# Optimization experiments

Measured on AMD Instinct MI355X. Metric: run time of the kernel, lower is better.

Reference implementation:

```python
import jax, jax.numpy as jnp
import numpy as np


def setup_inputs() -> dict:
    key = jax.random.key(0)
    ks = jax.random.split(key, 8)
    N, E = 100000, 3200000
    IN, H, OUT = 256, 128, 64
    x = jax.random.normal(ks[0], (N, IN), dtype=jnp.float32)
    src = jax.random.randint(ks[1], (E,), 0, N, dtype=jnp.int64)
    dst = jax.random.randint(ks[2], (E,), 0, N, dtype=jnp.int64)
    # Glorot-ish scaled weights
    W1_self = jax.random.normal(ks[3], (IN, H), dtype=jnp.float32) / np.sqrt(IN)
    W1_neigh = jax.random.normal(ks[4], (IN, H), dtype=jnp.float32) / np.sqrt(IN)
    b1 = jnp.zeros((H,), dtype=jnp.float32)
    W2_self = jax.random.normal(ks[5], (H, OUT), dtype=jnp.float32) / np.sqrt(H)
    W2_neigh = jax.random.normal(ks[6], (H, OUT), dtype=jnp.float32) / np.sqrt(H)
    b2 = jnp.zeros((OUT,), dtype=jnp.float32)
    return {"x": x, "src": src, "dst": dst,
            "W1_self": W1_self, "W1_neigh": W1_neigh, "b1": b1,
            "W2_self": W2_self, "W2_neigh": W2_neigh, "b2": b2}


def _sage_mean(h, src, dst, W_self, W_neigh, b, deg_inv):
    # mean aggregation over in-neighbors (edges src -> dst)
    N = h.shape[0]
    agg = jax.ops.segment_sum(h[src], dst, num_segments=N)  # [N, F]
    h_neigh = agg * deg_inv[:, None]
    return h @ W_self + h_neigh @ W_neigh + b


def reference(x, src, dst, W1_self, W1_neigh, b1, W2_self, W2_neigh, b2):
    N = x.shape[0]
    deg = jax.ops.segment_sum(jnp.ones_like(dst, dtype=x.dtype), dst, num_segments=N)
    deg_inv = 1.0 / jnp.maximum(deg, 1.0)  # DGL clamps in-degree to >= 1
    h = _sage_mean(x, src, dst, W1_self, W1_neigh, b1, deg_inv)
    h = jax.nn.relu(h)
    h = _sage_mean(h, src, dst, W2_self, W2_neigh, b2, deg_inv)
    return h
```

## Files before the change

kernel.cpp:

```cpp
#include <hip/hip_runtime.h>
#include <hip/hip_bf16.h>


typedef unsigned int uint32;
typedef __attribute__((ext_vector_type(8))) short short8;
typedef __attribute__((ext_vector_type(4))) float f32x4;

#define NBMAX 1024
#define EPB   8192

__device__ __forceinline__ unsigned short f2bf(float f) {
    unsigned u = __float_as_uint(f);
    u += 0x7fffu + ((u >> 16) & 1u);
    return (unsigned short)(u >> 16);
}
__device__ __forceinline__ uint32 pack2bf(float lo, float hi) {
    return (uint32)f2bf(lo) | ((uint32)f2bf(hi) << 16);
}
__device__ __forceinline__ float bf_lo(uint32 v) { return __uint_as_float(v << 16); }
__device__ __forceinline__ float bf_hi(uint32 v) { return __uint_as_float(v & 0xFFFF0000u); }

__global__ __launch_bounds__(256) void k_bucket_count(const int* __restrict__ dst, int E,
                                                      int* __restrict__ bcnt) {
    __shared__ int hist[NBMAX];
    for (int i = threadIdx.x; i < NBMAX; i += 256) hist[i] = 0;
    __syncthreads();
    int base = blockIdx.x * EPB;
    #pragma unroll 4
    for (int i = 0; i < EPB / 256; ++i) {
        int e = base + i * 256 + threadIdx.x;
        if (e < E) atomicAdd(&hist[dst[e] >> 7], 1);
    }
    __syncthreads();
    for (int i = threadIdx.x; i < NBMAX; i += 256) {
        int h = hist[i];
        if (h) atomicAdd(&bcnt[i], h);
    }
}

__global__ __launch_bounds__(1024) void k_bucket_scan(const int* __restrict__ bcnt, int NB,
                                                      int* __restrict__ boffs, int* __restrict__ gfill,
                                                      int E) {
    __shared__ int sd[1024];
    int tid = threadIdx.x;
    int v = (tid < NB) ? bcnt[tid] : 0;
    sd[tid] = v;
    __syncthreads();
    for (int off = 1; off < 1024; off <<= 1) {
        int t = (tid >= off) ? sd[tid - off] : 0;
        __syncthreads();
        sd[tid] += t;
        __syncthreads();
    }
    int excl = sd[tid] - v;
    if (tid < NB) { boffs[tid] = excl; gfill[tid] = excl; }
    if (tid == 0) boffs[NB] = E;
}

__global__ __launch_bounds__(256) void k_bucket_scatter(const int* __restrict__ src,
                                                        const int* __restrict__ dst, int E,
                                                        int* __restrict__ gfill,
                                                        uint32* __restrict__ pairs) {
    __shared__ int hist[NBMAX];
    __shared__ int basea[NBMAX];
    for (int i = threadIdx.x; i < NBMAX; i += 256) hist[i] = 0;
    __syncthreads();
    int base = blockIdx.x * EPB;
    #pragma unroll 4
    for (int i = 0; i < EPB / 256; ++i) {
        int e = base + i * 256 + threadIdx.x;
        if (e < E) atomicAdd(&hist[dst[e] >> 7], 1);
    }
    __syncthreads();
    for (int i = threadIdx.x; i < NBMAX; i += 256) {
        int h = hist[i];
        basea[i] = h ? atomicAdd(&gfill[i], h) : 0;
        hist[i] = 0;
    }
    __syncthreads();
    #pragma unroll 4
    for (int i = 0; i < EPB / 256; ++i) {
        int e = base + i * 256 + threadIdx.x;
        if (e < E) {
            int d = dst[e];
            int b = d >> 7;
            int pos = basea[b] + atomicAdd(&hist[b], 1);
            pairs[pos] = ((uint32)src[e] << 7) | (uint32)(d & 127);
        }
    }
}

__global__ __launch_bounds__(256) void k_bucket_sort(const uint32* __restrict__ pairs,
                                                     const int* __restrict__ boffs,
                                                     int N, int E,
                                                     int* __restrict__ row_start,
                                                     float* __restrict__ deg_inv,
                                                     int* __restrict__ src_sorted) {
    __shared__ int cnt[128];
    __shared__ int sc[128];
    __shared__ int fill[128];
    int b = blockIdx.x, tid = threadIdx.x;
    int s0 = boffs[b], s1 = boffs[b + 1];
    if (tid < 128) cnt[tid] = 0;
    __syncthreads();
    for (int e = s0 + tid; e < s1; e += 256)
        atomicAdd(&cnt[pairs[e] & 127], 1);
    __syncthreads();
    if (tid < 128) sc[tid] = cnt[tid];
    __syncthreads();
    for (int off = 1; off < 128; off <<= 1) {
        int v = 0;
        if (tid < 128 && tid >= off) v = sc[tid - off];
        __syncthreads();
        if (tid < 128) sc[tid] += v;
        __syncthreads();
    }
    if (tid < 128) {
        int excl = sc[tid] - cnt[tid];
        int node = b * 128 + tid;
        if (node < N) {
            row_start[node] = s0 + excl;
            int d = cnt[tid];
            deg_inv[node] = 1.0f / (float)(d > 1 ? d : 1);
        }
        fill[tid] = s0 + excl;
    }
    if (b == 0 && tid == 0) row_start[N] = E;
    __syncthreads();
    for (int e = s0 + tid; e < s1; e += 256) {
        uint32 p = pairs[e];
        int pos = atomicAdd(&fill[p & 127], 1);
        src_sorted[pos] = (int)(p >> 7);
    }
}

__global__ __launch_bounds__(256) void k_wt(const float* __restrict__ Ws, const float* __restrict__ Wn,
                                            int K, int logK, int halfC, unsigned short* __restrict__ Wt) {
    int t = blockIdx.x * blockDim.x + threadIdx.x;
    int total = 2 * halfC * K;
    if (t >= total) return;
    int c = t >> logK, k = t & (K - 1);
    float v = (c < halfC) ? Ws[(size_t)k * halfC + c] : Wn[(size_t)k * halfC + (c - halfC)];
    Wt[t] = f2bf(v);
}

template<int K, bool AF32, bool YSPLIT>
__global__ __launch_bounds__(256) void gemm_rs(const void* __restrict__ Aptr, int Arows, int nstrip,
                                               const unsigned short* __restrict__ Wt,
                                               unsigned short* __restrict__ P0,
                                               unsigned short* __restrict__ P1) {
    constexpr int KS = K / 32;
    __shared__ unsigned short Bs[128 * K];
    const int tid = threadIdx.x;
    const int wave = tid >> 6, lane = tid & 63;
    const int l15 = lane & 15, l4 = lane >> 4;

    const unsigned short* Wtblk = Wt + (YSPLIT ? (size_t)blockIdx.y * 128 * K : 0);
    unsigned short *dpA, *dpB; int ld;
    if (YSPLIT) { unsigned short* base = blockIdx.y ? P1 : P0; dpA = base; dpB = base + 64; ld = 128; }
    else        { dpA = P0; dpB = P1; ld = 64; }

    for (int i = tid; i < 16 * K; i += 256) {
        int col = i / (K / 8);
        int cb  = (i % (K / 8)) * 16;
        int sb  = cb ^ ((col & 7) << 4);
        uint4 v = *reinterpret_cast<const uint4*>(&Wtblk[(size_t)col * K + (cb >> 1)]);
        *reinterpret_cast<uint4*>(&Bs[col * K + (sb >> 1)]) = v;
    }
    __syncthreads();

    const int stride = gridDim.x;
    int g = blockIdx.x;
    if (g >= nstrip) return;

    float4 a[AF32 ? 2 * KS : 1];
    uint4  ub[AF32 ? 1 : KS];

    auto loadA = [&](int gg) {
        int arow = gg * 64 + wave * 16 + l15;
        if constexpr (AF32) {
            int r = arow < Arows ? arow : Arows - 1;
            const float* Ar = (const float*)Aptr + (size_t)r * K + l4 * 8;
            #pragma unroll
            for (int s = 0; s < KS; ++s) {
                a[2 * s]     = *reinterpret_cast<const float4*>(Ar + s * 32);
                a[2 * s + 1] = *reinterpret_cast<const float4*>(Ar + s * 32 + 4);
            }
        } else {
            const unsigned short* Ar = (const unsigned short*)Aptr + (size_t)arow * K + l4 * 8;
            #pragma unroll
            for (int s = 0; s < KS; ++s)
                ub[s] = *reinterpret_cast<const uint4*>(Ar + s * 32);
        }
    };

    loadA(g);
    while (true) {
        short8 af[KS];
        if constexpr (AF32) {
            #pragma unroll
            for (int s = 0; s < KS; ++s) {
                union { uint32 u[4]; short8 v; } cv;
                cv.u[0] = pack2bf(a[2*s].x,   a[2*s].y);
                cv.u[1] = pack2bf(a[2*s].z,   a[2*s].w);
                cv.u[2] = pack2bf(a[2*s+1].x, a[2*s+1].y);
                cv.u[3] = pack2bf(a[2*s+1].z, a[2*s+1].w);
                af[s] = cv.v;
            }
        } else {
            #pragma unroll
            for (int s = 0; s < KS; ++s) {
                union { uint4 q; short8 v; } cv;
                cv.q = ub[s];
                af[s] = cv.v;
            }
        }
        int gn = g + stride;
        if (gn < nstrip) loadA(gn);

        f32x4 acc[8] = {};
        #pragma unroll
        for (int s = 0; s < KS; ++s) {
            #pragma unroll
            for (int n = 0; n < 8; ++n) {
                int c = n * 16 + l15;
                int kb = s * 64 + l4 * 16;
                short8 bf = *reinterpret_cast<const short8*>(
                    &Bs[c * K + ((kb ^ ((c & 7) << 4)) >> 1)]);
                acc[n] = __builtin_amdgcn_mfma_f32_16x16x32_bf16(af[s], bf, acc[n], 0, 0, 0);
            }
        }
        const int rbase = g * 64 + wave * 16;
        #pragma unroll
        for (int n = 0; n < 8; ++n) {
            unsigned short* dp = (n < 4) ? dpA : dpB;
            int lc = (n & 3) * 16 + l15;
            #pragma unroll
            for (int r = 0; r < 4; ++r) {
                int rw = rbase + l4 * 4 + r;
                dp[(size_t)rw * ld + lc] = f2bf(acc[n][r]);
            }
        }
        if (gn >= nstrip) break;
        g = gn;
    }
}

__global__ __launch_bounds__(256) void k_agg1(const uint4* __restrict__ t1n, const uint4* __restrict__ t1s,
                                              const int* __restrict__ rs, const int* __restrict__ ss,
                                              const float* __restrict__ dinv, const float* __restrict__ b1,
                                              uint4* __restrict__ h, int N) {
    int wid  = (blockIdx.x * blockDim.x + threadIdx.x) >> 6;
    int lane = threadIdx.x & 63;
    if (wid >= N) return;
    int e0 = rs[wid], e1 = rs[wid + 1];
    const int q = lane >> 4, c = lane & 15;
    float a0 = 0, a1 = 0, a2 = 0, a3 = 0, a4 = 0, a5 = 0, a6 = 0, a7 = 0;
    int e = e0;
    for (; e + 16 <= e1; e += 16) {
        int s0 = ss[e + q];
        int s1 = ss[e + 4 + q];
        int s2 = ss[e + 8 + q];
        int s3 = ss[e + 12 + q];
        uint4 v0 = t1n[(size_t)s0 * 16 + c];
        uint4 v1 = t1n[(size_t)s1 * 16 + c];
        uint4 v2 = t1n[(size_t)s2 * 16 + c];
        uint4 v3 = t1n[(size_t)s3 * 16 + c];
        a0 += bf_lo(v0.x); a1 += bf_hi(v0.x); a2 += bf_lo(v0.y); a3 += bf_hi(v0.y);
        a4 += bf_lo(v0.z); a5 += bf_hi(v0.z); a6 += bf_lo(v0.w); a7 += bf_hi(v0.w);
        a0 += bf_lo(v1.x); a1 += bf_hi(v1.x); a2 += bf_lo(v1.y); a3 += bf_hi(v1.y);
        a4 += bf_lo(v1.z); a5 += bf_hi(v1.z); a6 += bf_lo(v1.w); a7 += bf_hi(v1.w);
        a0 += bf_lo(v2.x); a1 += bf_hi(v2.x); a2 += bf_lo(v2.y); a3 += bf_hi(v2.y);
        a4 += bf_lo(v2.z); a5 += bf_hi(v2.z); a6 += bf_lo(v2.w); a7 += bf_hi(v2.w);
        a0 += bf_lo(v3.x); a1 += bf_hi(v3.x); a2 += bf_lo(v3.y); a3 += bf_hi(v3.y);
        a4 += bf_lo(v3.z); a5 += bf_hi(v3.z); a6 += bf_lo(v3.w); a7 += bf_hi(v3.w);
    }
    for (; e < e1; e += 4) {
        if (e + q < e1) {
            int s = ss[e + q];
            uint4 v = t1n[(size_t)s * 16 + c];
            a0 += bf_lo(v.x); a1 += bf_hi(v.x); a2 += bf_lo(v.y); a3 += bf_hi(v.y);
            a4 += bf_lo(v.z); a5 += bf_hi(v.z); a6 += bf_lo(v.w); a7 += bf_hi(v.w);
        }
    }
    a0 += __shfl_xor(a0, 16); a1 += __shfl_xor(a1, 16); a2 += __shfl_xor(a2, 16); a3 += __shfl_xor(a3, 16);
    a4 += __shfl_xor(a4, 16); a5 += __shfl_xor(a5, 16); a6 += __shfl_xor(a6, 16); a7 += __shfl_xor(a7, 16);
    a0 += __shfl_xor(a0, 32); a1 += __shfl_xor(a1, 32); a2 += __shfl_xor(a2, 32); a3 += __shfl_xor(a3, 32);
    a4 += __shfl_xor(a4, 32); a5 += __shfl_xor(a5, 32); a6 += __shfl_xor(a6, 32); a7 += __shfl_xor(a7, 32);
    if (lane < 16) {
        float di = dinv[wid];
        uint4 sv = t1s[(size_t)wid * 16 + c];
        float4 bA = *reinterpret_cast<const float4*>(&b1[c * 8]);
        float4 bB = *reinterpret_cast<const float4*>(&b1[c * 8 + 4]);
        float h0 = fmaxf(fmaf(a0, di, bf_lo(sv.x)) + bA.x, 0.f);
        float h1 = fmaxf(fmaf(a1, di, bf_hi(sv.x)) + bA.y, 0.f);
        float h2 = fmaxf(fmaf(a2, di, bf_lo(sv.y)) + bA.z, 0.f);
        float h3 = fmaxf(fmaf(a3, di, bf_hi(sv.y)) + bA.w, 0.f);
        float h4 = fmaxf(fmaf(a4, di, bf_lo(sv.z)) + bB.x, 0.f);
        float h5 = fmaxf(fmaf(a5, di, bf_hi(sv.z)) + bB.y, 0.f);
        float h6 = fmaxf(fmaf(a6, di, bf_lo(sv.w)) + bB.z, 0.f);
        float h7 = fmaxf(fmaf(a7, di, bf_hi(sv.w)) + bB.w, 0.f);
        uint4 o;
        o.x = pack2bf(h0, h1); o.y = pack2bf(h2, h3);
        o.z = pack2bf(h4, h5); o.w = pack2bf(h6, h7);
        h[(size_t)wid * 16 + c] = o;
    }
}

__global__ __launch_bounds__(256) void k_agg2(const uint4* __restrict__ t2n, const uint4* __restrict__ t2s,
                                              const int* __restrict__ rs, const int* __restrict__ ss,
                                              const float* __restrict__ dinv, const float* __restrict__ b2,
                                              float* __restrict__ out, int N) {
    int wid  = (blockIdx.x * blockDim.x + threadIdx.x) >> 6;
    int lane = threadIdx.x & 63;
    if (wid >= N) return;
    int e0 = rs[wid], e1 = rs[wid + 1];
    const int o8 = lane >> 3, c = lane & 7;
    float a0 = 0, a1 = 0, a2 = 0, a3 = 0, a4 = 0, a5 = 0, a6 = 0, a7 = 0;
    int e = e0;
    for (; e + 32 <= e1; e += 32) {
        int s0 = ss[e + o8];
        int s1 = ss[e + 8 + o8];
        int s2 = ss[e + 16 + o8];
        int s3 = ss[e + 24 + o8];
        uint4 v0 = t2n[(size_t)s0 * 8 + c];
        uint4 v1 = t2n[(size_t)s1 * 8 + c];
        uint4 v2 = t2n[(size_t)s2 * 8 + c];
        uint4 v3 = t2n[(size_t)s3 * 8 + c];
        a0 += bf_lo(v0.x); a1 += bf_hi(v0.x); a2 += bf_lo(v0.y); a3 += bf_hi(v0.y);
        a4 += bf_lo(v0.z); a5 += bf_hi(v0.z); a6 += bf_lo(v0.w); a7 += bf_hi(v0.w);
        a0 += bf_lo(v1.x); a1 += bf_hi(v1.x); a2 += bf_lo(v1.y); a3 += bf_hi(v1.y);
        a4 += bf_lo(v1.z); a5 += bf_hi(v1.z); a6 += bf_lo(v1.w); a7 += bf_hi(v1.w);
        a0 += bf_lo(v2.x); a1 += bf_hi(v2.x); a2 += bf_lo(v2.y); a3 += bf_hi(v2.y);
        a4 += bf_lo(v2.z); a5 += bf_hi(v2.z); a6 += bf_lo(v2.w); a7 += bf_hi(v2.w);
        a0 += bf_lo(v3.x); a1 += bf_hi(v3.x); a2 += bf_lo(v3.y); a3 += bf_hi(v3.y);
        a4 += bf_lo(v3.z); a5 += bf_hi(v3.z); a6 += bf_lo(v3.w); a7 += bf_hi(v3.w);
    }
    for (; e < e1; e += 8) {
        if (e + o8 < e1) {
            int s = ss[e + o8];
            uint4 v = t2n[(size_t)s * 8 + c];
            a0 += bf_lo(v.x); a1 += bf_hi(v.x); a2 += bf_lo(v.y); a3 += bf_hi(v.y);
            a4 += bf_lo(v.z); a5 += bf_hi(v.z); a6 += bf_lo(v.w); a7 += bf_hi(v.w);
        }
    }
    a0 += __shfl_xor(a0, 8);  a1 += __shfl_xor(a1, 8);  a2 += __shfl_xor(a2, 8);  a3 += __shfl_xor(a3, 8);
    a4 += __shfl_xor(a4, 8);  a5 += __shfl_xor(a5, 8);  a6 += __shfl_xor(a6, 8);  a7 += __shfl_xor(a7, 8);
    a0 += __shfl_xor(a0, 16); a1 += __shfl_xor(a1, 16); a2 += __shfl_xor(a2, 16); a3 += __shfl_xor(a3, 16);
    a4 += __shfl_xor(a4, 16); a5 += __shfl_xor(a5, 16); a6 += __shfl_xor(a6, 16); a7 += __shfl_xor(a7, 16);
    a0 += __shfl_xor(a0, 32); a1 += __shfl_xor(a1, 32); a2 += __shfl_xor(a2, 32); a3 += __shfl_xor(a3, 32);
    a4 += __shfl_xor(a4, 32); a5 += __shfl_xor(a5, 32); a6 += __shfl_xor(a6, 32); a7 += __shfl_xor(a7, 32);
    if (lane < 8) {
        float di = dinv[wid];
        uint4 sv = t2s[(size_t)wid * 8 + c];
        float4 bA = *reinterpret_cast<const float4*>(&b2[c * 8]);
        float4 bB = *reinterpret_cast<const float4*>(&b2[c * 8 + 4]);
        float4 oA, oB;
        oA.x = fmaf(a0, di, bf_lo(sv.x)) + bA.x;
        oA.y = fmaf(a1, di, bf_hi(sv.x)) + bA.y;
        oA.z = fmaf(a2, di, bf_lo(sv.y)) + bA.z;
        oA.w = fmaf(a3, di, bf_hi(sv.y)) + bA.w;
        oB.x = fmaf(a4, di, bf_lo(sv.z)) + bB.x;
        oB.y = fmaf(a5, di, bf_hi(sv.z)) + bB.y;
        oB.z = fmaf(a6, di, bf_lo(sv.w)) + bB.z;
        oB.w = fmaf(a7, di, bf_hi(sv.w)) + bB.w;
        *reinterpret_cast<float4*>(&out[(size_t)wid * 64 + c * 8]) = oA;
        *reinterpret_cast<float4*>(&out[(size_t)wid * 64 + c * 8 + 4]) = oB;
    }
}

extern "C" void kernel_launch(void* const* d_in, const int* in_sizes, int n_in,
                              void* d_out, int out_size, void* d_ws, size_t ws_size,
                              hipStream_t stream) {
    const float* x   = (const float*)d_in[0];
    const int*   src = (const int*)d_in[1];
    const int*   dst = (const int*)d_in[2];
    const float* W1s = (const float*)d_in[3];
    const float* W1n = (const float*)d_in[4];
    const float* b1  = (const float*)d_in[5];
    const float* W2s = (const float*)d_in[6];
    const float* W2n = (const float*)d_in[7];
    const float* b2  = (const float*)d_in[8];
    float* out = (float*)d_out;

    const int IN = 256, H = 128, OUT = 64;
    const int N  = in_sizes[0] / IN;
    const int E  = in_sizes[1];
    const int Mpad = (N + 127) & ~127;
    const int NB = (N + 127) >> 7;

    char* ws = (char*)d_ws;
    size_t off = 0;
    auto alloc = [&](size_t bytes) -> char* {
        char* p = ws + off;
        off = (off + bytes + 255) & ~(size_t)255;
        return p;
    };
    int*   row_start  = (int*)  alloc((size_t)(N + 1) * 4);
    float* deg_inv    = (float*)alloc((size_t)N * 4);
    int*   bcnt       = (int*)  alloc((size_t)NBMAX * 4);
    int*   boffs      = (int*)  alloc((size_t)(NBMAX + 1) * 4);
    int*   gfill      = (int*)  alloc((size_t)NBMAX * 4);
    int*   src_sorted = (int*)  alloc((size_t)E * 4);
    uint32* pairs     = (uint32*)alloc((size_t)E * 4);
    unsigned short* Wt1 = (unsigned short*)alloc((size_t)(2 * H) * IN * 2);
    unsigned short* Wt2 = (unsigned short*)alloc((size_t)(2 * OUT) * H * 2);
    unsigned short* t1s = (unsigned short*)alloc((size_t)Mpad * H * 2);
    unsigned short* t1n = (unsigned short*)alloc((size_t)Mpad * H * 2);
    unsigned short* hbf = (unsigned short*)alloc((size_t)Mpad * H * 2);

    hipMemsetAsync(bcnt, 0, (size_t)NBMAX * 4, stream);
    int nblk = (E + EPB - 1) / EPB;
    k_bucket_count  <<<nblk, 256, 0, stream>>>(dst, E, bcnt);
    k_bucket_scan   <<<1, 1024, 0, stream>>>(bcnt, NB, boffs, gfill, E);
    k_bucket_scatter<<<nblk, 256, 0, stream>>>(src, dst, E, gfill, pairs);
    k_bucket_sort   <<<NB, 256, 0, stream>>>(pairs, boffs, N, E, row_start, deg_inv, src_sorted);

    k_wt<<<(2 * H * IN + 255) / 256, 256, 0, stream>>>(W1s, W1n, IN, 8, H, Wt1);
    k_wt<<<(2 * OUT * H + 255) / 256, 256, 0, stream>>>(W2s, W2n, H, 7, OUT, Wt2);

    int nstrip1 = (N + 63) / 64;
    gemm_rs<256, true, true><<<dim3(512, 2), 256, 0, stream>>>(x, N, nstrip1, Wt1, t1s, t1n);
    k_agg1<<<(N + 3) / 4, 256, 0, stream>>>((const uint4*)t1n, (const uint4*)t1s,
                                            row_start, src_sorted, deg_inv, b1, (uint4*)hbf, N);
    int nstrip2 = Mpad / 64;
    gemm_rs<128, false, false><<<dim3(512, 1), 256, 0, stream>>>(hbf, Mpad, nstrip2, Wt2, t1s, t1n);
    k_agg2<<<(N + 3) / 4, 256, 0, stream>>>((const uint4*)t1n, (const uint4*)t1s,
                                            row_start, src_sorted, deg_inv, b2, out, N);
}
```

Before: 364.9 us.

## Store neighbor-projected features in FP8 to halve gather traffic

The GEMM now writes the neighbor half of its projected output (h@W_neigh) as 8-bit floats, using hardware FP8 convert builtins when available and a software encoder otherwise. The self half stays in bf16. Both aggregation kernels gather 8-byte FP8 chunks instead of 16-byte bf16 chunks and decode them to fp32 before accumulating, which targets the dominant random-gather memory traffic over ~3.2M edges. The GEMM loop is also restructured into a double-buffered A-load ping-pong. The trade-off is reduced precision in the neighbor aggregates, which may affect accuracy tolerance.

```diff
diff --git a/kernel.cpp b/kernel.cpp
--- a/kernel.cpp
+++ b/kernel.cpp
@@ -8,6 +8,15 @@
 
 #define NBMAX 1024
 #define EPB   8192
+
+#if defined(__has_builtin)
+#if __has_builtin(__builtin_amdgcn_cvt_pk_f32_fp8) && __has_builtin(__builtin_amdgcn_cvt_pk_fp8_f32)
+#define FP8_HW 1
+#endif
+#endif
+#ifndef FP8_HW
+#define FP8_HW 0
+#endif
 
 __device__ __forceinline__ unsigned short f2bf(float f) {
     unsigned u = __float_as_uint(f);
@@ -19,6 +28,37 @@
 }
 __device__ __forceinline__ float bf_lo(uint32 v) { return __uint_as_float(v << 16); }
 __device__ __forceinline__ float bf_hi(uint32 v) { return __uint_as_float(v & 0xFFFF0000u); }
+
+__device__ __forceinline__ unsigned char enc8(float v) {
+#if FP8_HW
+    return (unsigned char)(__builtin_amdgcn_cvt_pk_fp8_f32(v, v, 0, false) & 0xFF);
+#else
+    float g = v * 0x1p-120f;
+    uint32 b = __float_as_uint(g);
+    uint32 s = (b >> 24) & 0x80u;
+    b &= 0x7fffffffu;
+    b += 0x7ffffu + ((b >> 20) & 1u);
+    int t = (int)(b >> 20) - 960;
+    t = t < 0 ? 0 : (t > 126 ? 126 : t);
+    return (unsigned char)(s | (uint32)t);
+#endif
+}
+#if !FP8_HW
+__device__ __forceinline__ float dec1(uint32 b) {
+    uint32 bits = ((b & 0x80u) << 24) | ((b & 0x7fu) << 20);
+    return __uint_as_float(bits) * 0x1p+120f;
+}
+#endif
+__device__ __forceinline__ void dec_u32(uint32 u, float& f0, float& f1, float& f2, float& f3) {
+#if FP8_HW
+    auto lo = __builtin_amdgcn_cvt_pk_f32_fp8(u, false);
+    auto hi = __builtin_amdgcn_cvt_pk_f32_fp8(u, true);
+    f0 = lo[0]; f1 = lo[1]; f2 = hi[0]; f3 = hi[1];
+#else
+    f0 = dec1(u & 0xffu); f1 = dec1((u >> 8) & 0xffu);
+    f2 = dec1((u >> 16) & 0xffu); f3 = dec1(u >> 24);
+#endif
+}
 
 __global__ __launch_bounds__(256) void k_bucket_count(const int* __restrict__ dst, int E,
                                                       int* __restrict__ bcnt) {
@@ -147,8 +187,8 @@
 template<int K, bool AF32, bool YSPLIT>
 __global__ __launch_bounds__(256) void gemm_rs(const void* __restrict__ Aptr, int Arows, int nstrip,
                                                const unsigned short* __restrict__ Wt,
-                                               unsigned short* __restrict__ P0,
-                                               unsigned short* __restrict__ P1) {
+                                               unsigned short* __restrict__ S16,
+                                               unsigned char* __restrict__ N8) {
     constexpr int KS = K / 32;
     __shared__ unsigned short Bs[128 * K];
     const int tid = threadIdx.x;
@@ -156,9 +196,7 @@
     const int l15 = lane & 15, l4 = lane >> 4;
 
     const unsigned short* Wtblk = Wt + (YSPLIT ? (size_t)blockIdx.y * 128 * K : 0);
-    unsigned short *dpA, *dpB; int ld;
-    if (YSPLIT) { unsigned short* base = blockIdx.y ? P1 : P0; dpA = base; dpB = base + 64; ld = 128; }
-    else        { dpA = P0; dpB = P1; ld = 64; }
+    const bool out8_all = YSPLIT && (blockIdx.y == 1);
 
     for (int i = tid; i < 16 * K; i += 256) {
         int col = i / (K / 8);
@@ -173,10 +211,10 @@
     int g = blockIdx.x;
     if (g >= nstrip) return;
 
-    float4 a[AF32 ? 2 * KS : 1];
-    uint4  ub[AF32 ? 1 : KS];
-
-    auto loadA = [&](int gg) {
+    float4 aA[AF32 ? 2 * KS : 1], aB[AF32 ? 2 * KS : 1];
+    uint4  uA[AF32 ? 1 : KS],     uB[AF32 ? 1 : KS];
+
+    auto loadA = [&](int gg, float4* a, uint4* ub) {
         int arow = gg * 64 + wave * 16 + l15;
         if constexpr (AF32) {
             int r = arow < Arows ? arow : Arows - 1;
@@ -194,8 +232,7 @@
         }
     };
 
-    loadA(g);
-    while (true) {
+    auto compute = [&](int gc, float4* a, uint4* ub) {
         short8 af[KS];
         if constexpr (AF32) {
             #pragma unroll
@@ -215,9 +252,6 @@
                 af[s] = cv.v;
             }
         }
-        int gn = g + stride;
-        if (gn < nstrip) loadA(gn);
-
         f32x4 acc[8] = {};
         #pragma unroll
         for (int s = 0; s < KS; ++s) {
@@ -230,23 +264,58 @@
                 acc[n] = __builtin_amdgcn_mfma_f32_16x16x32_bf16(af[s], bf, acc[n], 0, 0, 0);
             }
         }
-        const int rbase = g * 64 + wave * 16;
-        #pragma unroll
-        for (int n = 0; n < 8; ++n) {
-            unsigned short* dp = (n < 4) ? dpA : dpB;
-            int lc = (n & 3) * 16 + l15;
+        const int rbase = gc * 64 + wave * 16;
+        if constexpr (YSPLIT) {
+            if (out8_all) {
+                #pragma unroll
+                for (int n = 0; n < 8; ++n) {
+                    int col = n * 16 + l15;
+                    #pragma unroll
+                    for (int r = 0; r < 4; ++r) {
+                        int rw = rbase + l4 * 4 + r;
+                        N8[(size_t)rw * 128 + col] = enc8(acc[n][r]);
+                    }
+                }
+            } else {
+                #pragma unroll
+                for (int n = 0; n < 8; ++n) {
+                    int col = n * 16 + l15;
+                    #pragma unroll
+                    for (int r = 0; r < 4; ++r) {
+                        int rw = rbase + l4 * 4 + r;
+                        S16[(size_t)rw * 128 + col] = f2bf(acc[n][r]);
+                    }
+                }
+            }
+        } else {
             #pragma unroll
-            for (int r = 0; r < 4; ++r) {
-                int rw = rbase + l4 * 4 + r;
-                dp[(size_t)rw * ld + lc] = f2bf(acc[n][r]);
+            for (int n = 0; n < 8; ++n) {
+                #pragma unroll
+                for (int r = 0; r < 4; ++r) {
+                    int rw = rbase + l4 * 4 + r;
+                    if (n < 4) S16[(size_t)rw * 64 + n * 16 + l15] = f2bf(acc[n][r]);
+                    else       N8[(size_t)rw * 64 + (n - 4) * 16 + l15] = enc8(acc[n][r]);
+                }
             }
         }
+    };
+
+    loadA(g, aA, uA);
+    while (true) {
+        int gn = g + stride;
+        if (gn < nstrip) loadA(gn, aB, uB);
+        compute(g, aA, uA);
         if (gn >= nstrip) break;
         g = gn;
-    }
-}
-
-__global__ __launch_bounds__(256) void k_agg1(const uint4* __restrict__ t1n, const uint4* __restrict__ t1s,
+        gn = g + stride;
+        if (gn < nstrip) loadA(gn, aA, uA);
+        compute(g, aB, uB);
+        if (gn >= nstrip) break;
+        g = gn;
+    }
+}
+
+__global__ __launch_bounds__(256) void k_agg1(const uint2* __restrict__ t1n, const uint4* __restrict__ t1s,
                                               const int* __restrict__ rs, const int* __restrict__ ss,
                                               const float* __restrict__ dinv, const float* __restrict__ b1,
                                               uint4* __restrict__ h, int N) {
@@ -256,31 +325,32 @@
     int e0 = rs[wid], e1 = rs[wid + 1];
     const int q = lane >> 4, c = lane & 15;
     float a0 = 0, a1 = 0, a2 = 0, a3 = 0, a4 = 0, a5 = 0, a6 = 0, a7 = 0;
+    float f0, f1, f2, f3;
     int e = e0;
     for (; e + 16 <= e1; e += 16) {
         int s0 = ss[e + q];
         int s1 = ss[e + 4 + q];
         int s2 = ss[e + 8 + q];
         int s3 = ss[e + 12 + q];
-        uint4 v0 = t1n[(size_t)s0 * 16 + c];
-        uint4 v1 = t1n[(size_t)s1 * 16 + c];
-        uint4 v2 = t1n[(size_t)s2 * 16 + c];
-        uint4 v3 = t1n[(size_t)s3 * 16 + c];
-        a0 += bf_lo(v0.x); a1 += bf_hi(v0.x); a2 += bf_lo(v0.y); a3 += bf_hi(v0.y);
-        a4 += bf_lo(v0.z); a5 += bf_hi(v0.z); a6 += bf_lo(v0.w); a7 += bf_hi(v0.w);
-        a0 += bf_lo(v1.x); a1 += bf_hi(v1.x); a2 += bf_lo(v1.y); a3 += bf_hi(v1.y);
-        a4 += bf_lo(v1.z); a5 += bf_hi(v1.z); a6 += bf_lo(v1.w); a7 += bf_hi(v1.w);
-        a0 += bf_lo(v2.x); a1 += bf_hi(v2.x); a2 += bf_lo(v2.y); a3 += bf_hi(v2.y);
-        a4 += bf_lo(v2.z); a5 += bf_hi(v2.z); a6 += bf_lo(v2.w); a7 += bf_hi(v2.w);
-        a0 += bf_lo(v3.x); a1 += bf_hi(v3.x); a2 += bf_lo(v3.y); a3 += bf_hi(v3.y);
-        a4 += bf_lo(v3.z); a5 += bf_hi(v3.z); a6 += bf_lo(v3.w); a7 += bf_hi(v3.w);
+        uint2 v0 = t1n[(size_t)s0 * 16 + c];
+        uint2 v1 = t1n[(size_t)s1 * 16 + c];
+        uint2 v2 = t1n[(size_t)s2 * 16 + c];
+        uint2 v3 = t1n[(size_t)s3 * 16 + c];
+        dec_u32(v0.x, f0, f1, f2, f3); a0 += f0; a1 += f1; a2 += f2; a3 += f3;
+        dec_u32(v0.y, f0, f1, f2, f3); a4 += f0; a5 += f1; a6 += f2; a7 += f3;
+        dec_u32(v1.x, f0, f1, f2, f3); a0 += f0; a1 += f1; a2 += f2; a3 += f3;
+        dec_u32(v1.y, f0, f1, f2, f3); a4 += f0; a5 += f1; a6 += f2; a7 += f3;
+        dec_u32(v2.x, f0, f1, f2, f3); a0 += f0; a1 += f1; a2 += f2; a3 += f3;
+        dec_u32(v2.y, f0, f1, f2, f3); a4 += f0; a5 += f1; a6 += f2; a7 += f3;
+        dec_u32(v3.x, f0, f1, f2, f3); a0 += f0; a1 += f1; a2 += f2; a3 += f3;
+        dec_u32(v3.y, f0, f1, f2, f3); a4 += f0; a5 += f1; a6 += f2; a7 += f3;
     }
     for (; e < e1; e += 4) {
         if (e + q < e1) {
             int s = ss[e + q];
-            uint4 v = t1n[(size_t)s * 16 + c];
-            a0 += bf_lo(v.x); a1 += bf_hi(v.x); a2 += bf_lo(v.y); a3 += bf_hi(v.y);
-            a4 += bf_lo(v.z); a5 += bf_hi(v.z); a6 += bf_lo(v.w); a7 += bf_hi(v.w);
+            uint2 v = t1n[(size_t)s * 16 + c];
+            dec_u32(v.x, f0, f1, f2, f3); a0 += f0; a1 += f1; a2 += f2; a3 += f3;
+            dec_u32(v.y, f0, f1, f2, f3); a4 += f0; a5 += f1; a6 += f2; a7 += f3;
         }
     }
     a0 += __shfl_xor(a0, 16); a1 += __shfl_xor(a1, 16); a2 += __shfl_xor(a2, 16); a3 += __shfl_xor(a3, 16);
@@ -307,7 +377,7 @@
     }
 }
 
-__global__ __launch_bounds__(256) void k_agg2(const uint4* __restrict__ t2n, const uint4* __restrict__ t2s,
+__global__ __launch_bounds__(256) void k_agg2(const uint2* __restrict__ t2n, const uint4* __restrict__ t2s,
                                               const int* __restrict__ rs, const int* __restrict__ ss,
                                               const float* __restrict__ dinv, const float* __restrict__ b2,
                                               float* __restrict__ out, int N) {
@@ -317,31 +387,32 @@
     int e0 = rs[wid], e1 = rs[wid + 1];
     const int o8 = lane >> 3, c = lane & 7;
     float a0 = 0, a1 = 0, a2 = 0, a3 = 0, a4 = 0, a5 = 0, a6 = 0, a7 = 0;
+    float f0, f1, f2, f3;
     int e = e0;
     for (; e + 32 <= e1; e += 32) {
         int s0 = ss[e + o8];
         int s1 = ss[e + 8 + o8];
         int s2 = ss[e + 16 + o8];
         int s3 = ss[e + 24 + o8];
-        uint4 v0 = t2n[(size_t)s0 * 8 + c];
-        uint4 v1 = t2n[(size_t)s1 * 8 + c];
-        uint4 v2 = t2n[(size_t)s2 * 8 + c];
-        uint4 v3 = t2n[(size_t)s3 * 8 + c];
-        a0 += bf_lo(v0.x); a1 += bf_hi(v0.x); a2 += bf_lo(v0.y); a3 += bf_hi(v0.y);
-        a4 += bf_lo(v0.z); a5 += bf_hi(v0.z); a6 += bf_lo(v0.w); a7 += bf_hi(v0.w);
-        a0 += bf_lo(v1.x); a1 += bf_hi(v1.x); a2 += bf_lo(v1.y); a3 += bf_hi(v1.y);
-        a4 += bf_lo(v1.z); a5 += bf_hi(v1.z); a6 += bf_lo(v1.w); a7 += bf_hi(v1.w);
-        a0 += bf_lo(v2.x); a1 += bf_hi(v2.x); a2 += bf_lo(v2.y); a3 += bf_hi(v2.y);
-        a4 += bf_lo(v2.z); a5 += bf_hi(v2.z); a6 += bf_lo(v2.w); a7 += bf_hi(v2.w);
-        a0 += bf_lo(v3.x); a1 += bf_hi(v3.x); a2 += bf_lo(v3.y); a3 += bf_hi(v3.y);
-        a4 += bf_lo(v3.z); a5 += bf_hi(v3.z); a6 += bf_lo(v3.w); a7 += bf_hi(v3.w);
+        uint2 v0 = t2n[(size_t)s0 * 8 + c];
+        uint2 v1 = t2n[(size_t)s1 * 8 + c];
+        uint2 v2 = t2n[(size_t)s2 * 8 + c];
+        uint2 v3 = t2n[(size_t)s3 * 8 + c];
+        dec_u32(v0.x, f0, f1, f2, f3); a0 += f0; a1 += f1; a2 += f2; a3 += f3;
+        dec_u32(v0.y, f0, f1, f2, f3); a4 += f0; a5 += f1; a6 += f2; a7 += f3;
+        dec_u32(v1.x, f0, f1, f2, f3); a0 += f0; a1 += f1; a2 += f2; a3 += f3;
+        dec_u32(v1.y, f0, f1, f2, f3); a4 += f0; a5 += f1; a6 += f2; a7 += f3;
+        dec_u32(v2.x, f0, f1, f2, f3); a0 += f0; a1 += f1; a2 += f2; a3 += f3;
+        dec_u32(v2.y, f0, f1, f2, f3); a4 += f0; a5 += f1; a6 += f2; a7 += f3;
+        dec_u32(v3.x, f0, f1, f2, f3); a0 += f0; a1 += f1; a2 += f2; a3 += f3;
+        dec_u32(v3.y, f0, f1, f2, f3); a4 += f0; a5 += f1; a6 += f2; a7 += f3;
     }
     for (; e < e1; e += 8) {
         if (e + o8 < e1) {
             int s = ss[e + o8];
-            uint4 v = t2n[(size_t)s * 8 + c];
-            a0 += bf_lo(v.x); a1 += bf_hi(v.x); a2 += bf_lo(v.y); a3 += bf_hi(v.y);
-            a4 += bf_lo(v.z); a5 += bf_hi(v.z); a6 += bf_lo(v.w); a7 += bf_hi(v.w);
+            uint2 v = t2n[(size_t)s * 8 + c];
+            dec_u32(v.x, f0, f1, f2, f3); a0 += f0; a1 += f1; a2 += f2; a3 += f3;
+            dec_u32(v.y, f0, f1, f2, f3); a4 += f0; a5 += f1; a6 += f2; a7 += f3;
         }
     }
     a0 += __shfl_xor(a0, 8);  a1 += __shfl_xor(a1, 8);  a2 += __shfl_xor(a2, 8);  a3 += __shfl_xor(a3, 8);
@@ -406,7 +477,7 @@
     unsigned short* Wt1 = (unsigned short*)alloc((size_t)(2 * H) * IN * 2);
     unsigned short* Wt2 = (unsigned short*)alloc((size_t)(2 * OUT) * H * 2);
     unsigned short* t1s = (unsigned short*)alloc((size_t)Mpad * H * 2);
-    unsigned short* t1n = (unsigned short*)alloc((size_t)Mpad * H * 2);
+    unsigned char*  t1n = (unsigned char*) alloc((size_t)Mpad * H);
     unsigned short* hbf = (unsigned short*)alloc((size_t)Mpad * H * 2);
 
     hipMemsetAsync(bcnt, 0, (size_t)NBMAX * 4, stream);
@@ -421,10 +492,10 @@
 
     int nstrip1 = (N + 63) / 64;
     gemm_rs<256, true, true><<<dim3(512, 2), 256, 0, stream>>>(x, N, nstrip1, Wt1, t1s, t1n);
-    k_agg1<<<(N + 3) / 4, 256, 0, stream>>>((const uint4*)t1n, (const uint4*)t1s,
+    k_agg1<<<(N + 3) / 4, 256, 0, stream>>>((const uint2*)t1n, (const uint4*)t1s,
                                             row_start, src_sorted, deg_inv, b1, (uint4*)hbf, N);
     int nstrip2 = Mpad / 64;
     gemm_rs<128, false, false><<<dim3(512, 1), 256, 0, stream>>>(hbf, Mpad, nstrip2, Wt2, t1s, t1n);
-    k_agg2<<<(N + 3) / 4, 256, 0, stream>>>((const uint4*)t1n, (const uint4*)t1s,
+    k_agg2<<<(N + 3) / 4, 256, 0, stream>>>((const uint2*)t1n, (const uint4*)t1s,
                                             row_start, src_sorted, deg_inv, b2, out, N);
 }
```

After: 323.7 us. -11.3%, faster.
